# Kernel tuning notes

Measured on AMD Instinct MI355X. Metric: run time of the kernel, lower is better.

The kernel has to match this reference:

```python
import jax, jax.numpy as jnp
import numpy as np

B, NQ, NKV, D, H, HD = 8, 1024, 2048, 1024, 16, 64  # inner_dim = H*HD = 1024


def setup_inputs() -> dict:
    key = jax.random.key(0)
    ks = jax.random.split(key, 10)
    s = 0.02
    return {
        "latent": jax.random.normal(ks[0], (B, NQ, D), jnp.float32),
        "data": jax.random.normal(ks[1], (B, NKV, D), jnp.float32),
        "wq": jax.random.normal(ks[2], (D, H * HD), jnp.float32) * s,
        "bq": jax.random.normal(ks[3], (H * HD,), jnp.float32) * s,
        "wk": jax.random.normal(ks[4], (D, H * HD), jnp.float32) * s,
        "bk": jax.random.normal(ks[5], (H * HD,), jnp.float32) * s,
        "wv": jax.random.normal(ks[6], (D, H * HD), jnp.float32) * s,
        "bv": jax.random.normal(ks[7], (H * HD,), jnp.float32) * s,
        "wo": jax.random.normal(ks[8], (H * HD, D), jnp.float32) * s,
        "bo": jax.random.normal(ks[9], (D,), jnp.float32) * s,
    }


def reference(latent, data, wq, bq, wk, bk, wv, bv, wo, bo):
    scale = HD ** -0.5
    # projections: [b, n, H*HD] -> [b, h, n, d]
    def split_heads(t):
        b, n, _ = t.shape
        return t.reshape(b, n, H, HD).transpose(0, 2, 1, 3)

    q = split_heads(latent @ wq + bq)   # [b, h, nq, d]
    k = split_heads(data @ wk + bk)     # [b, h, nkv, d]
    v = split_heads(data @ wv + bv)     # [b, h, nkv, d]

    scores = jnp.einsum("bhid,bhjd->bhij", q, k) * scale  # [b, h, nq, nkv]
    att = jax.nn.softmax(scores, axis=-1)                  # dropout p=0 (eval)
    out = jnp.einsum("bhij,bhjd->bhid", att, v)            # [b, h, nq, d]
    out = out.transpose(0, 2, 1, 3).reshape(B, NQ, H * HD)
    return out @ wo + bo
```

## Files before the change

### kernel.cpp

```cpp
#include <hip/hip_runtime.h>
#include <hip/hip_bf16.h>
#include <math.h>


using short8  = __attribute__((ext_vector_type(8))) short;
using f32x4   = __attribute__((ext_vector_type(4))) float;
using uint4v  = __attribute__((ext_vector_type(4))) unsigned int;

__device__ __forceinline__ ushort f2bf(float f) {
    unsigned u = __builtin_bit_cast(unsigned, f);
    u = (u + 0x7FFFu + ((u >> 16) & 1u)) >> 16;
    return (ushort)u;
}
__device__ __forceinline__ unsigned pack_bf2(float lo, float hi) {
    unsigned ulo = __builtin_bit_cast(unsigned, lo) + 0x8000u;
    unsigned uhi = __builtin_bit_cast(unsigned, hi) + 0x8000u;
    return __builtin_amdgcn_perm(uhi, ulo, 0x07060302);
}

__device__ __forceinline__ void gld_lds16(const ushort* g, ushort* l) {
    __builtin_amdgcn_global_load_lds(
        (const __attribute__((address_space(1))) unsigned int*)(const void*)g,
        (__attribute__((address_space(3))) unsigned int*)(void*)l,
        16, 0, 0);
}

__global__ void cvt_bf16(const float* __restrict__ in, ushort* __restrict__ out, int n) {
    int i = (blockIdx.x * blockDim.x + threadIdx.x) * 8;
    if (i >= n) return;
    float4 a = *(const float4*)(in + i);
    float4 b = *(const float4*)(in + i + 4);
    short8 o;
    o[0] = (short)f2bf(a.x); o[1] = (short)f2bf(a.y);
    o[2] = (short)f2bf(a.z); o[3] = (short)f2bf(a.w);
    o[4] = (short)f2bf(b.x); o[5] = (short)f2bf(b.y);
    o[6] = (short)f2bf(b.z); o[7] = (short)f2bf(b.w);
    *(short8*)(out + i) = o;
}

__global__ void transpose_w(const float* __restrict__ w0, const float* __restrict__ w1,
                            const float* __restrict__ w2, const float* __restrict__ w3,
                            ushort* __restrict__ o0, ushort* __restrict__ o1,
                            ushort* __restrict__ o2, ushort* __restrict__ o3) {
    __shared__ ushort tile[32][33];
    int z = blockIdx.z;
    const float* in = (z == 0) ? w0 : (z == 1) ? w1 : (z == 2) ? w2 : w3;
    ushort* out     = (z == 0) ? o0 : (z == 1) ? o1 : (z == 2) ? o2 : o3;
    int tx = threadIdx.x, ty = threadIdx.y;
    int x = blockIdx.x * 32 + tx;
    int y = blockIdx.y * 32;
#pragma unroll
    for (int i = 0; i < 32; i += 8)
        tile[ty + i][tx] = f2bf(in[(size_t)(y + ty + i) * 1024 + x]);
    __syncthreads();
    int x2 = blockIdx.y * 32 + tx;
    int y2 = blockIdx.x * 32;
#pragma unroll
    for (int i = 0; i < 32; i += 8)
        out[(size_t)(y2 + ty + i) * 1024 + x2] = tile[tx][ty + i];
}

template <int S>
__device__ __forceinline__ void stage_half(const ushort* __restrict__ G, int rbase,
                                           ushort* tile, int H, int kcol,
                                           int wave, int lane) {
#pragma unroll
    for (int c = 0; c < 2; ++c) {
        int rho = c * 64 + wave * 8;
        int gr0 = (rho / S) * (2 * S) + H * S + (rho % S);
        int rig = lane >> 3;
        int q   = (lane & 7) ^ rig;
        gld_lds16(G + (size_t)(rbase + gr0 + rig) * 1024 + kcol + q * 8,
                  tile + gr0 * 64);
    }
}

__device__ __forceinline__ void gemm256_body(
        const ushort* __restrict__ A, const ushort* __restrict__ Bt,
        const float* __restrict__ bias, void* __restrict__ Cv,
        float scale, int mode, int bm, int bn) {
    __shared__ __align__(16) ushort sm[65536];
    ushort* As0 = sm;
    ushort* Bs0 = sm + 16384;
    ushort* As1 = sm + 32768;
    ushort* Bs1 = sm + 49152;

    const int tid  = threadIdx.x;
    const int wave = tid >> 6, lane = tid & 63;
    const int l15 = lane & 15, quad = lane >> 4;
    const int wm = wave >> 2, wn = wave & 3;
    const int m0 = bm * 256, n0 = bn * 256;

    const int rA  = wm * 128 + l15;
    const int rB  = wn * 64 + l15;
    const int cq0 = quad ^ (l15 & 7);
    const int cq1 = (4 + quad) ^ (l15 & 7);

    stage_half<64>(A,  m0, As0, 0, 0,  wave, lane);
    stage_half<32>(Bt, n0, Bs0, 0, 0,  wave, lane);
    stage_half<32>(Bt, n0, Bs0, 1, 0,  wave, lane);
    stage_half<64>(A,  m0, As0, 1, 0,  wave, lane);
    stage_half<64>(A,  m0, As1, 0, 64, wave, lane);
    stage_half<32>(Bt, n0, Bs1, 1, 64, wave, lane);
    stage_half<64>(A,  m0, As1, 1, 64, wave, lane);
    asm volatile("s_waitcnt vmcnt(6)" ::: "memory");
    __builtin_amdgcn_s_barrier();

    f32x4 acc[8][4] = {};

#define LDA(MH)                                                                   \
    _Pragma("unroll")                                                             \
    for (int mi = 0; mi < 4; ++mi) {                                              \
        a[mi][0] = *(const short8*)(Ac + (rA + (MH) * 64 + mi * 16) * 64 + cq0 * 8); \
        a[mi][1] = *(const short8*)(Ac + (rA + (MH) * 64 + mi * 16) * 64 + cq1 * 8); \
    }
#define LDB(NH)                                                                   \
    _Pragma("unroll")                                                             \
    for (int ni = 0; ni < 2; ++ni) {                                              \
        b[ni][0] = *(const short8*)(Bc + (rB + (NH) * 32 + ni * 16) * 64 + cq0 * 8); \
        b[ni][1] = *(const short8*)(Bc + (rB + (NH) * 32 + ni * 16) * 64 + cq1 * 8); \
    }
#define MFMA_PHASE(MB, NB)                                                        \
    __builtin_amdgcn_s_barrier();                                                 \
    asm volatile("s_waitcnt lgkmcnt(0)" ::: "memory");                            \
    __builtin_amdgcn_sched_barrier(0);                                            \
    __builtin_amdgcn_s_setprio(1);                                                \
    _Pragma("unroll")                                                             \
    for (int mi = 0; mi < 4; ++mi)                                                \
        _Pragma("unroll")                                                         \
        for (int ni = 0; ni < 2; ++ni)                                            \
            _Pragma("unroll")                                                     \
            for (int kk = 0; kk < 2; ++kk)                                        \
                acc[(MB) * 4 + mi][(NB) * 2 + ni] =                               \
                    __builtin_amdgcn_mfma_f32_16x16x32_bf16(                      \
                        a[mi][kk], b[ni][kk], acc[(MB) * 4 + mi][(NB) * 2 + ni],  \
                        0, 0, 0);                                                 \
    __builtin_amdgcn_s_setprio(0);                                                \
    __builtin_amdgcn_s_barrier();

#pragma unroll 2
    for (int g = 0; g < 16; ++g) {
        ushort* Ac = (g & 1) ? As1 : As0;
        ushort* Bc = (g & 1) ? Bs1 : Bs0;
        ushort* Bn = (g & 1) ? Bs0 : Bs1;
        const int k1 = ((g + 1) & 15) * 64;
        const int k2 = ((g + 2) & 15) * 64;
        short8 a[4][2], b[2][2];

        LDA(0) LDB(0)
        stage_half<32>(Bt, n0, Bn, 0, k1, wave, lane);
        MFMA_PHASE(0, 0)

        LDB(1)
        stage_half<64>(A, m0, Ac, 0, k2, wave, lane);
        MFMA_PHASE(0, 1)

        LDA(1)
        stage_half<32>(Bt, n0, Bc, 1, k2, wave, lane);
        MFMA_PHASE(1, 1)

        LDB(0)
        stage_half<64>(A, m0, Ac, 1, k2, wave, lane);
        asm volatile("s_waitcnt vmcnt(6)" ::: "memory");
        MFMA_PHASE(1, 0)
    }
#undef LDA
#undef LDB
#undef MFMA_PHASE

    asm volatile("s_waitcnt vmcnt(0)" ::: "memory");

    float bvv[4];
    int   cols[4];
#pragma unroll
    for (int n4 = 0; n4 < 4; ++n4) {
        cols[n4] = n0 + wn * 64 + n4 * 16 + l15;
        bvv[n4]  = bias[cols[n4]];
    }
#pragma unroll
    for (int m8 = 0; m8 < 8; ++m8) {
        int rbase = m0 + wm * 128 + m8 * 16 + quad * 4;
#pragma unroll
        for (int n4 = 0; n4 < 4; ++n4) {
            float v[4];
#pragma unroll
            for (int rr = 0; rr < 4; ++rr)
                v[rr] = (acc[m8][n4][rr] + bvv[n4]) * scale;
            if (mode == 1) {
                int kvl = rbase & 2047;
                int pos = (kvl & ~31) + ((kvl >> 2) & 3) * 8 + ((kvl >> 4) & 1) * 4;
                size_t base = ((size_t)((rbase >> 11) * 1024 + cols[n4])) * 2048 + pos;
                uint2 o;
                o.x = pack_bf2(v[0], v[1]);
                o.y = pack_bf2(v[2], v[3]);
                *(uint2*)((ushort*)Cv + base) = o;
            } else if (mode == 0) {
#pragma unroll
                for (int rr = 0; rr < 4; ++rr)
                    ((ushort*)Cv)[(size_t)(rbase + rr) * 1024 + cols[n4]] = f2bf(v[rr]);
            } else {
#pragma unroll
                for (int rr = 0; rr < 4; ++rr)
                    ((float*)Cv)[(size_t)(rbase + rr) * 1024 + cols[n4]] = v[rr];
            }
        }
    }
}

__global__ __launch_bounds__(512, 2) void proj_qkv(
        const ushort* __restrict__ latB, const ushort* __restrict__ datB,
        const ushort* __restrict__ wqT, const ushort* __restrict__ wkT,
        const ushort* __restrict__ wvT,
        const float* __restrict__ bq, const float* __restrict__ bk,
        const float* __restrict__ bv,
        ushort* __restrict__ Qb, ushort* __restrict__ Kb, ushort* __restrict__ Vtb,
        float qscale) {
    int bid = blockIdx.x;
    const ushort* A;
    const ushort* W;
    const float*  bias;
    void*         C;
    float sc;
    int mode, idx;
    if (bid < 128)      { A = latB; W = wqT; bias = bq; C = Qb;  sc = qscale; mode = 0; idx = bid; }
    else if (bid < 384) { A = datB; W = wkT; bias = bk; C = Kb;  sc = 1.f;    mode = 0; idx = bid - 128; }
    else                { A = datB; W = wvT; bias = bv; C = Vtb; sc = 1.f;    mode = 1; idx = bid - 384; }
    gemm256_body(A, W, bias, C, sc, mode, idx >> 2, idx & 3);
}

__global__ __launch_bounds__(512, 2) void gemm256_o(
        const ushort* __restrict__ A, const ushort* __restrict__ W,
        const float* __restrict__ bias, float* __restrict__ C) {
    gemm256_body(A, W, bias, C, 1.f, 2, (int)blockIdx.x >> 2, (int)blockIdx.x & 3);
}

__global__ __launch_bounds__(256, 4) void attn_fused(const ushort* __restrict__ Q,
                                                     const ushort* __restrict__ K,
                                                     const ushort* __restrict__ Vt,
                                                     ushort* __restrict__ O) {
    __shared__ __align__(16) ushort smem[2 * 8192];
    ushort* Ks  = smem;
    ushort* Vts = smem + 8192;

    const int tid  = threadIdx.x;
    const int wave = tid >> 6, lane = tid & 63;
    const int l15 = lane & 15, quad = lane >> 4;
    const int bx = blockIdx.x;
    const int bh = bx & 127, h = bh & 15, b = bh >> 4;
    const int q0 = (bx >> 7) * 128;

    const ushort* Qg = Q + ((size_t)(b * 1024 + q0)) * 1024 + h * 64;
    const ushort* Kg = K + ((size_t)(b * 2048)) * 1024 + h * 64;
    const ushort* Vg = Vt + ((size_t)(b * 1024 + h * 64)) * 2048;

    short8 bq[2][2];
#pragma unroll
    for (int qt = 0; qt < 2; ++qt) {
        int row = wave * 32 + qt * 16 + l15;
#pragma unroll
        for (int ks = 0; ks < 2; ++ks)
            bq[ks][qt] = *(const short8*)(Qg + (size_t)row * 1024 + ks * 32 + quad * 8);
    }

    f32x4 Oacc[4][2] = {};
    float l_run[2] = {0.f, 0.f};

    const int rig = lane >> 3;
    const int scb8 = (lane & 7) ^ rig;
    const int riv = lane >> 4;
    const int cb16 = lane & 15;

    for (int kv0 = 0; kv0 < 2048; kv0 += 128) {
        __syncthreads();
#pragma unroll
        for (int g = 0; g < 4; ++g) {
            int G = wave * 4 + g;
            gld_lds16(Kg + (size_t)(kv0 + G * 8 + rig) * 1024 + scb8 * 8, Ks + G * 512);
            int vrow = G * 4 + riv;
            int scv = cb16 ^ (vrow & 15);
            gld_lds16(Vg + (size_t)vrow * 2048 + kv0 + scv * 8, Vts + G * 512);
        }
        __syncthreads();

        unsigned pk[8][2][2];
#pragma unroll
        for (int kvt = 0; kvt < 8; ++kvt) {
            f32x4 s0 = {}, s1 = {};
#pragma unroll
            for (int ks = 0; ks < 2; ++ks) {
                int ck = ((ks * 4 + quad) ^ (l15 & 7)) * 8;
                short8 ak = *(const short8*)(Ks + (kvt * 16 + l15) * 64 + ck);
                s0 = __builtin_amdgcn_mfma_f32_16x16x32_bf16(ak, bq[ks][0], s0, 0, 0, 0);
                s1 = __builtin_amdgcn_mfma_f32_16x16x32_bf16(ak, bq[ks][1], s1, 0, 0, 0);
            }
            float p0[4], p1[4];
#pragma unroll
            for (int rr = 0; rr < 4; ++rr) {
                p0[rr] = __builtin_amdgcn_exp2f(s0[rr]);
                p1[rr] = __builtin_amdgcn_exp2f(s1[rr]);
                l_run[0] += p0[rr];
                l_run[1] += p1[rr];
            }
            pk[kvt][0][0] = pack_bf2(p0[0], p0[1]);
            pk[kvt][0][1] = pack_bf2(p0[2], p0[3]);
            pk[kvt][1][0] = pack_bf2(p1[0], p1[1]);
            pk[kvt][1][1] = pack_bf2(p1[2], p1[3]);
        }

#pragma unroll
        for (int sp = 0; sp < 4; ++sp) {
#pragma unroll
            for (int dt = 0; dt < 4; ++dt) {
                int cv = ((sp * 4 + quad) ^ l15) * 8;
                short8 av = *(const short8*)(Vts + (dt * 16 + l15) * 128 + cv);
#pragma unroll
                for (int qt = 0; qt < 2; ++qt) {
                    uint4v u = {pk[2 * sp][qt][0], pk[2 * sp][qt][1],
                                pk[2 * sp + 1][qt][0], pk[2 * sp + 1][qt][1]};
                    short8 bp = __builtin_bit_cast(short8, u);
                    Oacc[dt][qt] = __builtin_amdgcn_mfma_f32_16x16x32_bf16(av, bp, Oacc[dt][qt], 0, 0, 0);
                }
            }
        }
    }

#pragma unroll
    for (int qt = 0; qt < 2; ++qt) {
        float l = l_run[qt];
        l += __shfl_xor(l, 16);
        l += __shfl_xor(l, 32);
        float inv = 1.f / l;
        int qg = q0 + wave * 32 + qt * 16 + l15;
#pragma unroll
        for (int dt = 0; dt < 4; ++dt) {
            uint2 o;
            o.x = pack_bf2(Oacc[dt][qt][0] * inv, Oacc[dt][qt][1] * inv);
            o.y = pack_bf2(Oacc[dt][qt][2] * inv, Oacc[dt][qt][3] * inv);
            *(uint2*)(O + ((size_t)(b * 1024 + qg)) * 1024 + h * 64 + dt * 16 + quad * 4) = o;
        }
    }
}

extern "C" void kernel_launch(void* const* d_in, const int* in_sizes, int n_in,
                              void* d_out, int out_size, void* d_ws, size_t ws_size,
                              hipStream_t stream) {
    const float* latent = (const float*)d_in[0];
    const float* data   = (const float*)d_in[1];
    const float* wq     = (const float*)d_in[2];
    const float* bq     = (const float*)d_in[3];
    const float* wk     = (const float*)d_in[4];
    const float* bk     = (const float*)d_in[5];
    const float* wv     = (const float*)d_in[6];
    const float* bv     = (const float*)d_in[7];
    const float* wo     = (const float*)d_in[8];
    const float* bo     = (const float*)d_in[9];
    float* out = (float*)d_out;

    ushort* ws   = (ushort*)d_ws;
    ushort* wqT  = ws;
    ushort* wkT  = wqT + (1u << 20);
    ushort* wvT  = wkT + (1u << 20);
    ushort* woT  = wvT + (1u << 20);
    ushort* latB = woT + (1u << 20);
    ushort* datB = latB + (8u << 20);
    ushort* Qb   = datB + (16u << 20);
    ushort* Kb   = Qb + (8u << 20);
    ushort* Vtb  = Kb + (16u << 20);
    ushort* AO   = Vtb + (16u << 20);

    cvt_bf16<<<(8u << 20) / (256 * 8), 256, 0, stream>>>(latent, latB, 8u << 20);
    cvt_bf16<<<(16u << 20) / (256 * 8), 256, 0, stream>>>(data, datB, 16u << 20);
    transpose_w<<<dim3(32, 32, 4), dim3(32, 8), 0, stream>>>(wq, wk, wv, wo, wqT, wkT, wvT, woT);

    const float qscale = 0.125f * 1.44269504088896340736f;
    proj_qkv<<<dim3(640), 512, 0, stream>>>(latB, datB, wqT, wkT, wvT,
                                            bq, bk, bv, Qb, Kb, Vtb, qscale);
    attn_fused<<<dim3(1024), 256, 0, stream>>>(Qb, Kb, Vtb, AO);
    gemm256_o<<<dim3(128), 512, 0, stream>>>(AO, woT, bo, out);
}
```

Before: 392.5 us.

## Swizzle QKV projection block order and use 128x128 tile GEMM for output projection

The projection kernel's block index is remapped so that consecutive hardware block IDs are interleaved across the Q, K and V work ranges, which changes how blocks spread across XCDs and caches. The output projection moves from 128 large 256-tile blocks to a new 128x128-tile GEMM kernel with 512 blocks, aiming for better CU occupancy on a 256-CU device. The new kernel is simple and single-buffered, with a K step of 32 and a sync per step, so per-block efficiency may be lower.

```diff
diff --git a/kernel.cpp b/kernel.cpp
--- a/kernel.cpp
+++ b/kernel.cpp
@@ -215,7 +215,7 @@
         const float* __restrict__ bv,
         ushort* __restrict__ Qb, ushort* __restrict__ Kb, ushort* __restrict__ Vtb,
         float qscale) {
-    int bid = blockIdx.x;
+    int bid = ((int)blockIdx.x & 7) * 80 + ((int)blockIdx.x >> 3);
     const ushort* A;
     const ushort* W;
     const float*  bias;
@@ -228,10 +228,82 @@
     gemm256_body(A, W, bias, C, sc, mode, idx >> 2, idx & 3);
 }
 
-__global__ __launch_bounds__(512, 2) void gemm256_o(
-        const ushort* __restrict__ A, const ushort* __restrict__ W,
-        const float* __restrict__ bias, float* __restrict__ C) {
-    gemm256_body(A, W, bias, C, 1.f, 2, (int)blockIdx.x >> 2, (int)blockIdx.x & 3);
+template <int MODE>
+__global__ void gemm_bt(const ushort* __restrict__ A, const ushort* __restrict__ Bt,
+                        const float* __restrict__ bias, void* __restrict__ Cv,
+                        int K, float scale) {
+    __shared__ __align__(16) ushort As[128 * 32];
+    __shared__ __align__(16) ushort Bs[128 * 32];
+    const int tid  = threadIdx.x;
+    const int wave = tid >> 6, lane = tid & 63;
+    const int l15 = lane & 15, quad = lane >> 4;
+    const int wm = wave & 1, wn = wave >> 1;
+    const int m0 = blockIdx.x * 128;
+    const int n0 = blockIdx.y * 128;
+
+    f32x4 acc[4][4] = {};
+
+    for (int k0 = 0; k0 < K; k0 += 32) {
+        __syncthreads();
+#pragma unroll
+        for (int i = 0; i < 2; ++i) {
+            int f   = (i * 256 + tid) * 8;
+            int row = f >> 5, col = f & 31;
+            gld_lds16(A  + (size_t)(m0 + row) * K + k0 + col, As + (i * 256 + wave * 64) * 8);
+            gld_lds16(Bt + (size_t)(n0 + row) * K + k0 + col, Bs + (i * 256 + wave * 64) * 8);
+        }
+        __syncthreads();
+
+        short8 a[4], b[4];
+#pragma unroll
+        for (int mi = 0; mi < 4; ++mi)
+            a[mi] = *(const short8*)(As + (wm * 64 + mi * 16 + l15) * 32 + quad * 8);
+#pragma unroll
+        for (int ni = 0; ni < 4; ++ni)
+            b[ni] = *(const short8*)(Bs + (wn * 64 + ni * 16 + l15) * 32 + quad * 8);
+#pragma unroll
+        for (int mi = 0; mi < 4; ++mi)
+#pragma unroll
+            for (int ni = 0; ni < 4; ++ni)
+                acc[mi][ni] = __builtin_amdgcn_mfma_f32_16x16x32_bf16(a[mi], b[ni], acc[mi][ni], 0, 0, 0);
+    }
+
+    float bv[4];
+    int   cols[4];
+#pragma unroll
+    for (int ni = 0; ni < 4; ++ni) {
+        cols[ni] = n0 + wn * 64 + ni * 16 + l15;
+        bv[ni]   = bias[cols[ni]];
+    }
+#pragma unroll
+    for (int mi = 0; mi < 4; ++mi) {
+        int rbase = m0 + wm * 64 + mi * 16 + quad * 4;
+#pragma unroll
+        for (int ni = 0; ni < 4; ++ni) {
+            float v[4];
+#pragma unroll
+            for (int rr = 0; rr < 4; ++rr)
+                v[rr] = (acc[mi][ni][rr] + bv[ni]) * scale;
+            if (MODE == 1) {
+                int kvl = rbase & 2047;
+                int pos = (kvl & ~31) + ((kvl >> 2) & 3) * 8 + ((kvl >> 4) & 1) * 4;
+                size_t base = ((size_t)((rbase >> 11) * 1024 + cols[ni])) * 2048 + pos;
+                uint2 o;
+                o.x = pack_bf2(v[0], v[1]);
+                o.y = pack_bf2(v[2], v[3]);
+                *(uint2*)((ushort*)Cv + base) = o;
+            } else {
+#pragma unroll
+                for (int rr = 0; rr < 4; ++rr) {
+                    int row = rbase + rr;
+                    if (MODE == 0)
+                        ((ushort*)Cv)[(size_t)row * 1024 + cols[ni]] = f2bf(v[rr]);
+                    else
+                        ((float*)Cv)[(size_t)row * 1024 + cols[ni]] = v[rr];
+                }
+            }
+        }
+    }
 }
 
 __global__ __launch_bounds__(256, 4) void attn_fused(const ushort* __restrict__ Q,
@@ -376,5 +448,5 @@
     proj_qkv<<<dim3(640), 512, 0, stream>>>(latB, datB, wqT, wkT, wvT,
                                             bq, bk, bv, Qb, Kb, Vtb, qscale);
     attn_fused<<<dim3(1024), 256, 0, stream>>>(Qb, Kb, Vtb, AO);
-    gemm256_o<<<dim3(128), 512, 0, stream>>>(AO, woT, bo, out);
-}
+    gemm_bt<2><<<dim3(64, 8), 256, 0, stream>>>(AO, woT, bo, out, 1024, 1.0f);
+}
```

New measurement: 364.1 us. -7.2%, faster.
